# Kernel tuning notes

Hardware: AMD Instinct MI355X
Metric: run time of the kernel (lower is better)

The kernel has to match this reference:

```python
import jax, jax.numpy as jnp
import numpy as np

L, M, K, N = 131072, 511, 512, 512
STRIDE = (L - N) // (M - 1)  # 256; stride*(M-1)+N == L
B = 128
KH = K // 2 + 1  # 257 one-sided bins


def _tukey(n_pts, alpha=0.25):
    # scipy.signal.windows.tukey, sym=True
    n = np.arange(n_pts, dtype=np.float64)
    edge = alpha * (n_pts - 1) / 2.0
    w = np.ones(n_pts)
    left = n < edge
    w[left] = 0.5 * (1.0 + np.cos(np.pi * (2.0 * n[left] / (alpha * (n_pts - 1)) - 1.0)))
    right = n > (n_pts - 1) - edge
    w[right] = 0.5 * (1.0 + np.cos(np.pi * (2.0 * n[right] / (alpha * (n_pts - 1)) - 2.0 / alpha + 1.0)))
    return w


def _make_consts():
    w = _tukey(N, 0.25)
    w = (w / w.sum()).astype(np.float32)
    # fourier_matrix[n, k] = exp(-2*pi*i/N)**(n*k), sliced to K//2+1 cols, * sqrt(N)
    nk = np.outer(np.arange(N, dtype=np.float64), np.arange(K, dtype=np.float64))
    sigma = np.exp(-2j * np.pi / N)
    fm = (sigma ** nk)[:, :KH] * np.sqrt(N)
    return jnp.asarray(w), jnp.asarray(fm.astype(np.complex64))


def setup_inputs() -> dict:
    key = jax.random.key(0)
    x = jax.random.normal(key, (B, L), dtype=jnp.float32)
    window, fourier_matrix = _make_consts()
    return {"x": x, "window": window, "fourier_matrix": fourier_matrix}


def reference(x, window, fourier_matrix):
    xc = x.astype(jnp.complex64)
    xc = xc - jnp.mean(xc, axis=1, keepdims=True)
    # unfold(1, N, STRIDE) -> [B, M, N] overlapping frames
    idx = jnp.arange(M)[:, None] * STRIDE + jnp.arange(N)[None, :]  # [M, N]
    frames = xc[:, idx] * window[None, None, :].astype(jnp.complex64)  # [B, M, N]
    spec = jnp.matmul(frames, fourier_matrix)  # [B, M, KH] complex
    return jnp.abs(spec)
```

## Files before the change

kernel.cpp:

```cpp
#include <hip/hip_runtime.h>
#include <math.h>

#define L_LEN    131072
#define M_FRAMES 511
#define N_FFT    512
#define KH       257
#define FSTRIDE  256
#define B_BATCH  128

#define TM       32
#define RSTRIDE  36
#define SQRT_N   22.62741699796952f

__device__ __forceinline__ float hw_sin_rev(float rev) {
    float r; asm("v_sin_f32 %0, %1" : "=v"(r) : "v"(rev)); return r;
}
__device__ __forceinline__ float hw_cos_rev(float rev) {
    float r; asm("v_cos_f32 %0, %1" : "=v"(r) : "v"(rev)); return r;
}

__global__ __launch_bounds__(1024) void mean_kernel(const float* __restrict__ x,
                                                    float* __restrict__ means) {
    const int b = blockIdx.x;
    const float4* row = (const float4*)(x + (size_t)b * L_LEN);
    float s = 0.f;
    const int nvec = L_LEN / 4;
    for (int i = threadIdx.x; i < nvec; i += 1024) {
        float4 v = row[i];
        s += (v.x + v.y) + (v.z + v.w);
    }
    for (int off = 32; off > 0; off >>= 1) s += __shfl_down(s, off, 64);
    __shared__ float wsum[16];
    const int wid = threadIdx.x >> 6, lane = threadIdx.x & 63;
    if (lane == 0) wsum[wid] = s;
    __syncthreads();
    if (threadIdx.x == 0) {
        float t = 0.f;
        #pragma unroll
        for (int i = 0; i < 16; ++i) t += wsum[i];
        means[b] = t / (float)L_LEN;
    }
}

__global__ __launch_bounds__(256) void spec_kernel(const float* __restrict__ x,
                                                   const float* __restrict__ w,
                                                   const float* __restrict__ means,
                                                   float* __restrict__ out) {
    __shared__ __align__(16) float lds[256 * RSTRIDE * 2 + 512 + 256];
    float* Es  = lds;
    float* Os  = lds + 256 * RSTRIDE;
    float* wl  = lds + 512 * RSTRIDE;
    float* nyq = wl + 512;

    const int b  = blockIdx.x;
    const int m0 = blockIdx.y * TM;
    const int t  = threadIdx.x;
    const float mean = means[b];

    wl[t]       = w[t];
    wl[t + 256] = w[t + 256];
    __syncthreads();

    {
        const int n = t;
        const float* xb = x + (size_t)b * L_LEN + (size_t)m0 * FSTRIDE;
        for (int f = 0; f < TM; ++f) {
            float Ev = 0.f, Ov = 0.f;
            if (m0 + f < M_FRAMES) {
                const float* xf = xb + f * FSTRIDE;
                if (n == 0) {
                    Ev = SQRT_N * ((xf[0]   - mean) * wl[0]);
                    Ov = SQRT_N * ((xf[256] - mean) * wl[256]);
                } else {
                    float a = (xf[n]       - mean) * wl[n];
                    float c = (xf[512 - n] - mean) * wl[512 - n];
                    Ev = SQRT_N * (a + c);
                    Ov = SQRT_N * (a - c);
                }
            }
            Es[n * RSTRIDE + f] = Ev;
            Os[n * RSTRIDE + f] = Ov;
        }
    }
    __syncthreads();

    const int kg = t & 63;
    const int fg = t >> 6;
    const float* Er = Es + 8 * fg;
    const float* Or = Os + 8 * fg;

    float re[4][8], im[4][8];

    {
        const float sgn = (kg & 1) ? -1.f : 1.f;
        float4 e0a = *(const float4*)(Er);
        float4 e0b = *(const float4*)(Er + 4);
        float4 o0a = *(const float4*)(Or);
        float4 o0b = *(const float4*)(Or + 4);
        float e0[8] = {e0a.x, e0a.y, e0a.z, e0a.w, e0b.x, e0b.y, e0b.z, e0b.w};
        float o0[8] = {o0a.x, o0a.y, o0a.z, o0a.w, o0b.x, o0b.y, o0b.z, o0b.w};
        #pragma unroll
        for (int u = 0; u < 4; ++u)
            #pragma unroll
            for (int ff = 0; ff < 8; ++ff) {
                re[u][ff] = fmaf(sgn, o0[ff], e0[ff]);
                im[u][ff] = 0.f;
            }
    }

    float ck[4], sk[4];
    #pragma unroll
    for (int u = 0; u < 4; ++u) {
        float rev = (float)(kg + 64 * u) * (1.0f / 512.0f);
        ck[u] = hw_cos_rev(rev);
        sk[u] = hw_sin_rev(rev);
    }

    #pragma unroll 1
    for (int seg = 0; seg < 4; ++seg) {
        const int n0   = seg ? seg * 64 : 1;
        const int nend = seg * 64 + 64;
        float c[4], s[4];
        #pragma unroll
        for (int u = 0; u < 4; ++u) {
            int p = (n0 * (kg + 64 * u)) & 511;
            float rev = (float)p * (1.0f / 512.0f);
            c[u] = hw_cos_rev(rev);
            s[u] = hw_sin_rev(rev);
        }
        for (int n = n0; n < nend; ++n) {
            const float* er = Er + n * RSTRIDE;
            const float* orr = Or + n * RSTRIDE;
            float4 ea = *(const float4*)er;
            float4 eb = *(const float4*)(er + 4);
            float4 oa = *(const float4*)orr;
            float4 ob = *(const float4*)(orr + 4);
            #pragma unroll
            for (int u = 0; u < 4; ++u) {
                re[u][0] = fmaf(ea.x, c[u], re[u][0]);  im[u][0] = fmaf(oa.x, s[u], im[u][0]);
                re[u][1] = fmaf(ea.y, c[u], re[u][1]);  im[u][1] = fmaf(oa.y, s[u], im[u][1]);
                re[u][2] = fmaf(ea.z, c[u], re[u][2]);  im[u][2] = fmaf(oa.z, s[u], im[u][2]);
                re[u][3] = fmaf(ea.w, c[u], re[u][3]);  im[u][3] = fmaf(oa.w, s[u], im[u][3]);
                re[u][4] = fmaf(eb.x, c[u], re[u][4]);  im[u][4] = fmaf(ob.x, s[u], im[u][4]);
                re[u][5] = fmaf(eb.y, c[u], re[u][5]);  im[u][5] = fmaf(ob.y, s[u], im[u][5]);
                re[u][6] = fmaf(eb.z, c[u], re[u][6]);  im[u][6] = fmaf(ob.z, s[u], im[u][6]);
                re[u][7] = fmaf(eb.w, c[u], re[u][7]);  im[u][7] = fmaf(ob.w, s[u], im[u][7]);
                float t1 = s[u] * sk[u];
                float t2 = s[u] * ck[u];
                float cn = fmaf(c[u], ck[u], -t1);
                float sn = fmaf(c[u], sk[u],  t2);
                c[u] = cn; s[u] = sn;
            }
        }
    }

    #pragma unroll
    for (int u = 0; u < 4; ++u)
        #pragma unroll
        for (int ff = 0; ff < 8; ++ff) {
            const int f = fg * 8 + ff;
            if (m0 + f < M_FRAMES) {
                float r = re[u][ff], i2 = im[u][ff];
                out[((size_t)b * M_FRAMES + (m0 + f)) * KH + kg + 64 * u] =
                    sqrtf(fmaf(r, r, i2 * i2));
            }
        }

    {
        const int g = t >> 5, f = t & 31;
        float acc = 0.f;
        const int nlo = g * 32;
        for (int n2 = nlo; n2 < nlo + 32; n2 += 2) {
            acc += Es[n2 * RSTRIDE + f] - Es[(n2 + 1) * RSTRIDE + f];
        }
        nyq[g * 32 + f] = acc;
    }
    __syncthreads();
    if (t < 32) {
        const int f = t;
        if (m0 + f < M_FRAMES) {
            float acc = Os[f];
            #pragma unroll
            for (int g = 0; g < 8; ++g) acc += nyq[g * 32 + f];
            out[((size_t)b * M_FRAMES + (m0 + f)) * KH + 256] = fabsf(acc);
        }
    }
}

extern "C" void kernel_launch(void* const* d_in, const int* in_sizes, int n_in,
                              void* d_out, int out_size, void* d_ws, size_t ws_size,
                              hipStream_t stream) {
    const float* x = (const float*)d_in[0];
    const float* w = (const float*)d_in[1];
    float* out   = (float*)d_out;
    float* means = (float*)d_ws;

    mean_kernel<<<dim3(B_BATCH), dim3(1024), 0, stream>>>(x, means);

    const int mtiles = (M_FRAMES + TM - 1) / TM;
    spec_kernel<<<dim3(B_BATCH, mtiles), dim3(256), 0, stream>>>(x, w, means, out);
}
```

Before: 371.6 us.

## Use packed FP32 FMA in DFT loop and split mean into partial sums

The inner DFT accumulation now uses v_pk_fma_f32 and v_pk_mul_f32 over pairs of frames, which halves the VALU instruction count for the multiply-accumulates and the twiddle rotation. The mean reduction becomes 1024 blocks that each write a partial sum, and spec_kernel adds the eight partials itself, so the reduction spreads over more CUs. spec_kernel also gets launch_bounds(256,2) and a 2x unroll. The risks are register pressure from the duplicated twiddle vectors and inline asm limiting how the compiler schedules the loop.

After: 370.4 us. No clear change (-0.3%).

```diff
diff --git a/kernel.cpp b/kernel.cpp
--- a/kernel.cpp
+++ b/kernel.cpp
@@ -12,40 +12,38 @@
 #define RSTRIDE  36
 #define SQRT_N   22.62741699796952f
 
-__device__ __forceinline__ float hw_sin_rev(float rev) {
-    float r; asm("v_sin_f32 %0, %1" : "=v"(r) : "v"(rev)); return r;
-}
-__device__ __forceinline__ float hw_cos_rev(float rev) {
-    float r; asm("v_cos_f32 %0, %1" : "=v"(r) : "v"(rev)); return r;
-}
-
-__global__ __launch_bounds__(1024) void mean_kernel(const float* __restrict__ x,
-                                                    float* __restrict__ means) {
-    const int b = blockIdx.x;
-    const float4* row = (const float4*)(x + (size_t)b * L_LEN);
+typedef float pkf2 __attribute__((ext_vector_type(2)));
+
+__device__ __forceinline__ pkf2 pk_fma(pkf2 a, pkf2 b, pkf2 c) {
+    pkf2 d; asm("v_pk_fma_f32 %0, %1, %2, %3" : "=v"(d) : "v"(a), "v"(b), "v"(c)); return d;
+}
+__device__ __forceinline__ pkf2 pk_mul(pkf2 a, pkf2 b) {
+    pkf2 d; asm("v_pk_mul_f32 %0, %1, %2" : "=v"(d) : "v"(a), "v"(b)); return d;
+}
+__device__ __forceinline__ float hw_sin_rev(float rev){float r;asm("v_sin_f32 %0, %1":"=v"(r):"v"(rev));return r;}
+__device__ __forceinline__ float hw_cos_rev(float rev){float r;asm("v_cos_f32 %0, %1":"=v"(r):"v"(rev));return r;}
+
+__global__ __launch_bounds__(256) void pmean_kernel(const float* __restrict__ x,
+                                                    float* __restrict__ partial) {
+    const int b = blockIdx.x >> 3, chunk = blockIdx.x & 7;
+    const float4* p = (const float4*)(x + (size_t)b * L_LEN + (size_t)chunk * (L_LEN / 8));
     float s = 0.f;
-    const int nvec = L_LEN / 4;
-    for (int i = threadIdx.x; i < nvec; i += 1024) {
-        float4 v = row[i];
+    const int nvec = L_LEN / 8 / 4;
+    for (int i = threadIdx.x; i < nvec; i += 256) {
+        float4 v = p[i];
         s += (v.x + v.y) + (v.z + v.w);
     }
-    for (int off = 32; off > 0; off >>= 1) s += __shfl_down(s, off, 64);
-    __shared__ float wsum[16];
-    const int wid = threadIdx.x >> 6, lane = threadIdx.x & 63;
-    if (lane == 0) wsum[wid] = s;
-    __syncthreads();
-    if (threadIdx.x == 0) {
-        float t = 0.f;
-        #pragma unroll
-        for (int i = 0; i < 16; ++i) t += wsum[i];
-        means[b] = t / (float)L_LEN;
-    }
-}
-
-__global__ __launch_bounds__(256) void spec_kernel(const float* __restrict__ x,
-                                                   const float* __restrict__ w,
-                                                   const float* __restrict__ means,
-                                                   float* __restrict__ out) {
+    for (int off = 32; off; off >>= 1) s += __shfl_down(s, off, 64);
+    __shared__ float ws[4];
+    if ((threadIdx.x & 63) == 0) ws[threadIdx.x >> 6] = s;
+    __syncthreads();
+    if (threadIdx.x == 0) partial[blockIdx.x] = (ws[0] + ws[1]) + (ws[2] + ws[3]);
+}
+
+__global__ __launch_bounds__(256, 2) void spec_kernel(const float* __restrict__ x,
+                                                      const float* __restrict__ w,
+                                                      const float* __restrict__ partial,
+                                                      float* __restrict__ out) {
     __shared__ __align__(16) float lds[256 * RSTRIDE * 2 + 512 + 256];
     float* Es  = lds;
     float* Os  = lds + 256 * RSTRIDE;
@@ -55,7 +53,11 @@
     const int b  = blockIdx.x;
     const int m0 = blockIdx.y * TM;
     const int t  = threadIdx.x;
-    const float mean = means[b];
+
+    float msum = 0.f;
+    #pragma unroll
+    for (int i = 0; i < 8; ++i) msum += partial[(b << 3) + i];
+    const float mean = msum * (1.0f / (float)L_LEN);
 
     wl[t]       = w[t];
     wl[t + 256] = w[t + 256];
@@ -89,82 +91,89 @@
     const float* Er = Es + 8 * fg;
     const float* Or = Os + 8 * fg;
 
-    float re[4][8], im[4][8];
+    pkf2 re2[4][4], im2[4][4];
 
     {
-        const float sgn = (kg & 1) ? -1.f : 1.f;
-        float4 e0a = *(const float4*)(Er);
-        float4 e0b = *(const float4*)(Er + 4);
-        float4 o0a = *(const float4*)(Or);
-        float4 o0b = *(const float4*)(Or + 4);
-        float e0[8] = {e0a.x, e0a.y, e0a.z, e0a.w, e0b.x, e0b.y, e0b.z, e0b.w};
-        float o0[8] = {o0a.x, o0a.y, o0a.z, o0a.w, o0b.x, o0b.y, o0b.z, o0b.w};
+        const float sg = (kg & 1) ? -1.f : 1.f;
+        pkf2 sg2 = {sg, sg};
         #pragma unroll
-        for (int u = 0; u < 4; ++u)
-            #pragma unroll
-            for (int ff = 0; ff < 8; ++ff) {
-                re[u][ff] = fmaf(sgn, o0[ff], e0[ff]);
-                im[u][ff] = 0.f;
-            }
-    }
-
-    float ck[4], sk[4];
+        for (int j = 0; j < 4; ++j) {
+            pkf2 e0 = *(const pkf2*)(Er + 2 * j);
+            pkf2 o0 = *(const pkf2*)(Or + 2 * j);
+            pkf2 r0 = pk_fma(sg2, o0, e0);
+            #pragma unroll
+            for (int u = 0; u < 4; ++u) { re2[u][j] = r0; im2[u][j] = (pkf2){0.f, 0.f}; }
+        }
+    }
+
+    pkf2 ck2[4], sk2[4], msk2[4];
     #pragma unroll
     for (int u = 0; u < 4; ++u) {
         float rev = (float)(kg + 64 * u) * (1.0f / 512.0f);
-        ck[u] = hw_cos_rev(rev);
-        sk[u] = hw_sin_rev(rev);
+        float ck = hw_cos_rev(rev), sk = hw_sin_rev(rev);
+        ck2[u]  = (pkf2){ck, ck};
+        sk2[u]  = (pkf2){sk, sk};
+        msk2[u] = (pkf2){-sk, -sk};
     }
 
     #pragma unroll 1
     for (int seg = 0; seg < 4; ++seg) {
         const int n0   = seg ? seg * 64 : 1;
         const int nend = seg * 64 + 64;
-        float c[4], s[4];
+        pkf2 c2[4], s2[4];
         #pragma unroll
         for (int u = 0; u < 4; ++u) {
             int p = (n0 * (kg + 64 * u)) & 511;
             float rev = (float)p * (1.0f / 512.0f);
-            c[u] = hw_cos_rev(rev);
-            s[u] = hw_sin_rev(rev);
-        }
+            float c = hw_cos_rev(rev), s = hw_sin_rev(rev);
+            c2[u] = (pkf2){c, c};
+            s2[u] = (pkf2){s, s};
+        }
+        #pragma unroll 2
         for (int n = n0; n < nend; ++n) {
-            const float* er = Er + n * RSTRIDE;
-            const float* orr = Or + n * RSTRIDE;
-            float4 ea = *(const float4*)er;
-            float4 eb = *(const float4*)(er + 4);
-            float4 oa = *(const float4*)orr;
-            float4 ob = *(const float4*)(orr + 4);
+            const float* ern = Er + n * RSTRIDE;
+            const float* orn = Or + n * RSTRIDE;
+            pkf2 e2[4], o2[4];
+            #pragma unroll
+            for (int j = 0; j < 4; ++j) {
+                e2[j] = *(const pkf2*)(ern + 2 * j);
+                o2[j] = *(const pkf2*)(orn + 2 * j);
+            }
             #pragma unroll
             for (int u = 0; u < 4; ++u) {
-                re[u][0] = fmaf(ea.x, c[u], re[u][0]);  im[u][0] = fmaf(oa.x, s[u], im[u][0]);
-                re[u][1] = fmaf(ea.y, c[u], re[u][1]);  im[u][1] = fmaf(oa.y, s[u], im[u][1]);
-                re[u][2] = fmaf(ea.z, c[u], re[u][2]);  im[u][2] = fmaf(oa.z, s[u], im[u][2]);
-                re[u][3] = fmaf(ea.w, c[u], re[u][3]);  im[u][3] = fmaf(oa.w, s[u], im[u][3]);
-                re[u][4] = fmaf(eb.x, c[u], re[u][4]);  im[u][4] = fmaf(ob.x, s[u], im[u][4]);
-                re[u][5] = fmaf(eb.y, c[u], re[u][5]);  im[u][5] = fmaf(ob.y, s[u], im[u][5]);
-                re[u][6] = fmaf(eb.z, c[u], re[u][6]);  im[u][6] = fmaf(ob.z, s[u], im[u][6]);
-                re[u][7] = fmaf(eb.w, c[u], re[u][7]);  im[u][7] = fmaf(ob.w, s[u], im[u][7]);
-                float t1 = s[u] * sk[u];
-                float t2 = s[u] * ck[u];
-                float cn = fmaf(c[u], ck[u], -t1);
-                float sn = fmaf(c[u], sk[u],  t2);
-                c[u] = cn; s[u] = sn;
+                re2[u][0] = pk_fma(e2[0], c2[u], re2[u][0]);
+                im2[u][0] = pk_fma(o2[0], s2[u], im2[u][0]);
+                re2[u][1] = pk_fma(e2[1], c2[u], re2[u][1]);
+                im2[u][1] = pk_fma(o2[1], s2[u], im2[u][1]);
+                re2[u][2] = pk_fma(e2[2], c2[u], re2[u][2]);
+                im2[u][2] = pk_fma(o2[2], s2[u], im2[u][2]);
+                re2[u][3] = pk_fma(e2[3], c2[u], re2[u][3]);
+                im2[u][3] = pk_fma(o2[3], s2[u], im2[u][3]);
+                pkf2 ta = pk_mul(c2[u], ck2[u]);
+                pkf2 tb = pk_mul(c2[u], sk2[u]);
+                c2[u] = pk_fma(s2[u], msk2[u], ta);
+                s2[u] = pk_fma(s2[u], ck2[u],  tb);
             }
         }
     }
 
     #pragma unroll
-    for (int u = 0; u < 4; ++u)
+    for (int u = 0; u < 4; ++u) {
         #pragma unroll
-        for (int ff = 0; ff < 8; ++ff) {
-            const int f = fg * 8 + ff;
-            if (m0 + f < M_FRAMES) {
-                float r = re[u][ff], i2 = im[u][ff];
-                out[((size_t)b * M_FRAMES + (m0 + f)) * KH + kg + 64 * u] =
-                    sqrtf(fmaf(r, r, i2 * i2));
-            }
-        }
+        for (int j = 0; j < 4; ++j) {
+            const int f0 = fg * 8 + 2 * j;
+            if (m0 + f0 < M_FRAMES) {
+                float r = re2[u][j].x, ii = im2[u][j].x;
+                out[((size_t)b * M_FRAMES + (m0 + f0)) * KH + kg + 64 * u] =
+                    sqrtf(fmaf(r, r, ii * ii));
+            }
+            if (m0 + f0 + 1 < M_FRAMES) {
+                float r = re2[u][j].y, ii = im2[u][j].y;
+                out[((size_t)b * M_FRAMES + (m0 + f0 + 1)) * KH + kg + 64 * u] =
+                    sqrtf(fmaf(r, r, ii * ii));
+            }
+        }
+    }
 
     {
         const int g = t >> 5, f = t & 31;
@@ -192,11 +201,11 @@
                               hipStream_t stream) {
     const float* x = (const float*)d_in[0];
     const float* w = (const float*)d_in[1];
-    float* out   = (float*)d_out;
-    float* means = (float*)d_ws;
-
-    mean_kernel<<<dim3(B_BATCH), dim3(1024), 0, stream>>>(x, means);
+    float* out     = (float*)d_out;
+    float* partial = (float*)d_ws;
+
+    pmean_kernel<<<dim3(B_BATCH * 8), dim3(256), 0, stream>>>(x, partial);
 
     const int mtiles = (M_FRAMES + TM - 1) / TM;
-    spec_kernel<<<dim3(B_BATCH, mtiles), dim3(256), 0, stream>>>(x, w, means, out);
-}
+    spec_kernel<<<dim3(B_BATCH, mtiles), dim3(256), 0, stream>>>(x, w, partial, out);
+}
```
